# Kernel optimization log

Hardware: AMD Instinct MI355X
Metric: run time of the kernel (lower is better)

Reference implementation:

```python
import jax, jax.numpy as jnp
import numpy as np

N = 50000   # num_nodes
E = 800000  # num_edges (avg degree 16)
IN, H, OUT = 256, 128, 64
L = 4       # num_layers


def setup_inputs() -> dict:
    key = jax.random.key(0)
    ks = jax.random.split(key, 6)
    x = jax.random.normal(ks[0], (N, IN), jnp.float32)
    edge_index = jax.random.randint(ks[1], (2, E), 0, N, dtype=jnp.int64)
    W1 = jax.random.normal(ks[2], (IN, H), jnp.float32) / np.float32(np.sqrt(IN))
    b1 = jnp.zeros((H,), jnp.float32)
    Wr = jax.random.normal(ks[3], (L, H, H), jnp.float32) / np.float32(np.sqrt(H))
    eps = jnp.zeros((L,), jnp.float32)  # epsilons init to 0 as in the module
    W2 = jax.random.normal(ks[4], (H, OUT), jnp.float32) / np.float32(np.sqrt(H))
    b2 = jnp.zeros((OUT,), jnp.float32)
    return {"x": x, "W1": W1, "b1": b1, "Wr": Wr, "eps": eps,
            "W2": W2, "b2": b2, "edge_index": edge_index}


def reference(x, W1, b1, Wr, eps, W2, b2, edge_index):
    n = x.shape[0]
    # add self loops (done once in __init__ of the torch module)
    sl = jnp.arange(n, dtype=edge_index.dtype)
    row = jnp.concatenate([edge_index[0], sl])
    col = jnp.concatenate([edge_index[1], sl])
    # sym-normalized adjacency A_hat = D^-1/2 (A + I) D^-1/2; L_sym = I - A_hat
    deg = jax.ops.segment_sum(jnp.ones(row.shape, x.dtype), row, num_segments=n)
    dinv = jnp.where(deg > 0, jax.lax.rsqrt(deg), jnp.zeros_like(deg))
    w = dinv[row] * dinv[col]  # [E+N]

    def ahat(h):  # A_hat @ h via gather + segment scatter-add
        return jax.ops.segment_sum(w[:, None] * h[col], row, num_segments=n)

    h = jax.nn.relu(x @ W1 + b1)  # lin1 + ReLU (dropout = identity at eval)
    h0 = h
    for layer in range(Wr.shape[0]):
        h = h @ Wr[layer].T                 # lin_right (bias-free)
        h = 6.0 * h - 3.0 * ahat(h)         # 3 * (I + L_sym) @ h
        h0 = (1.0 + jnp.tanh(eps[layer])) * h0 + h  # epsilon-gated residual
        h = jax.nn.relu(h0)
    return h @ W2 + b2  # lin2 logits
```

## Files before the change

kernel.cpp:

```cpp
#include <hip/hip_runtime.h>
#include <math.h>


#define GBLK 256

typedef __bf16 bf16x8 __attribute__((ext_vector_type(8)));
typedef float f32x4 __attribute__((ext_vector_type(4)));
typedef unsigned int uint32x4 __attribute__((ext_vector_type(4)));

__device__ __forceinline__ ushort f2bf(float f) {
  unsigned u = __float_as_uint(f);
  return (ushort)((u + 0x7fffu + ((u >> 16) & 1u)) >> 16);
}

__global__ void k_count(const int* __restrict__ eidx, int* __restrict__ degi, int E, int n) {
  int e = blockIdx.x * blockDim.x + threadIdx.x;
  if (e < E) {
    int r = eidx[e];
    if ((unsigned)r < (unsigned)n) atomicAdd(&degi[r], 1);
  }
}

__global__ __launch_bounds__(1024) void k_scan1(const int* __restrict__ degi,
                                                int* __restrict__ rowstart,
                                                int* __restrict__ bsum, int n) {
  __shared__ int sm[1024];
  int tid = threadIdx.x;
  int i = blockIdx.x * 1024 + tid;
  int v = (i < n) ? degi[i] : 0;
  sm[tid] = v;
  __syncthreads();
  #pragma unroll
  for (int off = 1; off < 1024; off <<= 1) {
    int t = (tid >= off) ? sm[tid - off] : 0;
    __syncthreads();
    sm[tid] += t;
    __syncthreads();
  }
  if (i < n) rowstart[i] = sm[tid] - v;
  if (tid == 1023) bsum[blockIdx.x] = sm[1023];
}

__global__ void k_scan2(const int* __restrict__ bsum, int* __restrict__ boff, int nb) {
  if (threadIdx.x == 0 && blockIdx.x == 0) {
    int s = 0;
    for (int b = 0; b < nb; ++b) { boff[b] = s; s += bsum[b]; }
  }
}

__global__ __launch_bounds__(1024) void k_scan3(int* __restrict__ rowstart,
                                                const int* __restrict__ boff,
                                                int* __restrict__ cursor, int n, int E) {
  int i = blockIdx.x * 1024 + threadIdx.x;
  if (i < n) {
    int v = rowstart[i] + boff[blockIdx.x];
    rowstart[i] = v;
    cursor[i] = v;
  }
  if (i == 0) rowstart[n] = E;
}

__global__ void k_dinv(const int* __restrict__ degi, float* __restrict__ dinv, int n) {
  int i = blockIdx.x * blockDim.x + threadIdx.x;
  if (i < n) dinv[i] = rsqrtf((float)degi[i] + 1.0f);
}

__global__ void k_fill(const int* __restrict__ eidx, int* __restrict__ cursor,
                       int* __restrict__ colidx, int E, int n) {
  int e = blockIdx.x * blockDim.x + threadIdx.x;
  if (e < E) {
    int r = eidx[e];
    int c = eidx[E + e];
    if ((unsigned)r < (unsigned)n && (unsigned)c < (unsigned)n) {
      int pos = atomicAdd(&cursor[r], 1);
      colidx[pos] = c;
    }
  }
}

__global__ void k_cvt(const float* __restrict__ Wr, const float* __restrict__ W1,
                      const float* __restrict__ W2, ushort* __restrict__ wr_bf,
                      ushort* __restrict__ w1t, ushort* __restrict__ w2t,
                      int nwr, int nw1, int nw2) {
  int i = blockIdx.x * blockDim.x + threadIdx.x;
  if (i < nwr) {
    wr_bf[i] = f2bf(Wr[i]);
  } else if (i < nwr + nw1) {
    int m = i - nwr;
    int k = m >> 7, j = m & 127;
    w1t[j * 256 + k] = f2bf(W1[m]);
  } else if (i < nwr + nw1 + nw2) {
    int m = i - nwr - nw1;
    int k = m >> 6, j = m & 63;
    w2t[j * 128 + k] = f2bf(W2[m]);
  }
}

template <int K, int NOUT, bool AF32, int EPI>
__global__ __launch_bounds__(256) void mfma_gemm(const void* __restrict__ Ap,
                                                 const ushort* __restrict__ Bt,
                                                 const float* __restrict__ bias,
                                                 const float* __restrict__ dinv,
                                                 ushort* __restrict__ out_bf,
                                                 float* __restrict__ out_f32,
                                                 int n) {
  constexpr int KS = K / 32;
  constexpr int NT = NOUT / 16;
  const int lane = threadIdx.x & 63;
  const int wave = threadIdx.x >> 6;
  const int l15 = lane & 15;
  const int kq = lane >> 4;
  const int rowA = blockIdx.x * 64 + wave * 16 + l15;
  const bool arow_ok = rowA < n;

  f32x4 acc[NT];
  #pragma unroll
  for (int t = 0; t < NT; ++t) acc[t] = (f32x4){0.f, 0.f, 0.f, 0.f};

  #pragma unroll
  for (int kk = 0; kk < KS; ++kk) {
    bf16x8 a;
    if constexpr (AF32) {
      const float* A = (const float*)Ap;
      float4 f0 = make_float4(0.f, 0.f, 0.f, 0.f);
      float4 f1 = make_float4(0.f, 0.f, 0.f, 0.f);
      if (arow_ok) {
        f0 = *(const float4*)&A[(size_t)rowA * K + kk * 32 + kq * 8];
        f1 = *(const float4*)&A[(size_t)rowA * K + kk * 32 + kq * 8 + 4];
      }
      uint32x4 u;
      u[0] = (unsigned)f2bf(f0.x) | ((unsigned)f2bf(f0.y) << 16);
      u[1] = (unsigned)f2bf(f0.z) | ((unsigned)f2bf(f0.w) << 16);
      u[2] = (unsigned)f2bf(f1.x) | ((unsigned)f2bf(f1.y) << 16);
      u[3] = (unsigned)f2bf(f1.z) | ((unsigned)f2bf(f1.w) << 16);
      a = __builtin_bit_cast(bf16x8, u);
    } else {
      const ushort* A = (const ushort*)Ap;
      uint32x4 u = (uint32x4){0u, 0u, 0u, 0u};
      if (arow_ok) u = *(const uint32x4*)&A[(size_t)rowA * K + kk * 32 + kq * 8];
      a = __builtin_bit_cast(bf16x8, u);
    }
    #pragma unroll
    for (int t = 0; t < NT; ++t) {
      uint32x4 ub = *(const uint32x4*)&Bt[(size_t)(t * 16 + l15) * K + kk * 32 + kq * 8];
      bf16x8 b = __builtin_bit_cast(bf16x8, ub);
      acc[t] = __builtin_amdgcn_mfma_f32_16x16x32_bf16(a, b, acc[t], 0, 0, 0);
    }
  }

  const int rbase = blockIdx.x * 64 + wave * 16 + kq * 4;

  float bcol[NT];
  #pragma unroll
  for (int t = 0; t < NT; ++t) {
    if constexpr (EPI != 1) bcol[t] = bias[t * 16 + l15];
    else bcol[t] = 0.f;
  }
  float sc[4];
  #pragma unroll
  for (int r = 0; r < 4; ++r) {
    if constexpr (EPI == 1) sc[r] = (rbase + r < n) ? dinv[rbase + r] : 0.f;
    else sc[r] = 0.f;
  }

  #pragma unroll
  for (int r = 0; r < 4; ++r) {
    int row = rbase + r;
    if (row < n) {
      #pragma unroll
      for (int t = 0; t < NT; ++t) {
        int col = t * 16 + l15;
        float v = acc[t][r];
        if constexpr (EPI == 0) {
          v += bcol[t];
          v = fmaxf(v, 0.f);
          out_bf[(size_t)row * NOUT + col] = f2bf(v);
          out_f32[(size_t)row * NOUT + col] = v;
        } else if constexpr (EPI == 1) {
          out_bf[(size_t)row * NOUT + col] = f2bf(v * sc[r]);
        } else {
          out_f32[(size_t)row * NOUT + col] = v + bcol[t];
        }
      }
    }
  }
}

__global__ __launch_bounds__(256) void k_spmm2(const ushort* __restrict__ pre,
                                               const float* __restrict__ dinv,
                                               const int* __restrict__ rowstart,
                                               const int* __restrict__ colidx,
                                               const float* __restrict__ eps, int layer,
                                               float* __restrict__ h0,
                                               ushort* __restrict__ hbf, int n) {
  const int lane = threadIdx.x & 63;
  const int r = blockIdx.x * 4 + (threadIdx.x >> 6);
  if (r >= n) return;

  const int s0 = rowstart[r], s1 = rowstart[r + 1];
  const float dr = dinv[r];

  const size_t rowoff = (size_t)r * 128 + lane * 2;
  const unsigned ur = *(const unsigned*)&pre[rowoff];
  const float2 h0v = *(const float2*)&h0[rowoff];

  float accx = 0.f, accy = 0.f;
  for (int base = s0; base < s1; base += 64) {
    int m = s1 - base; if (m > 64) m = 64;
    int ci = 0;
    if (base + lane < s1) ci = colidx[base + lane];
    int e = 0;
    for (; e + 3 < m; e += 4) {
      int c0 = __shfl(ci, e);
      int c1 = __shfl(ci, e + 1);
      int c2 = __shfl(ci, e + 2);
      int c3 = __shfl(ci, e + 3);
      unsigned u0 = *(const unsigned*)&pre[(size_t)c0 * 128 + lane * 2];
      unsigned u1 = *(const unsigned*)&pre[(size_t)c1 * 128 + lane * 2];
      unsigned u2 = *(const unsigned*)&pre[(size_t)c2 * 128 + lane * 2];
      unsigned u3 = *(const unsigned*)&pre[(size_t)c3 * 128 + lane * 2];
      accx += __uint_as_float(u0 << 16);
      accy += __uint_as_float(u0 & 0xffff0000u);
      accx += __uint_as_float(u1 << 16);
      accy += __uint_as_float(u1 & 0xffff0000u);
      accx += __uint_as_float(u2 << 16);
      accy += __uint_as_float(u2 & 0xffff0000u);
      accx += __uint_as_float(u3 << 16);
      accy += __uint_as_float(u3 & 0xffff0000u);
    }
    for (; e < m; ++e) {
      int c = __shfl(ci, e);
      unsigned u = *(const unsigned*)&pre[(size_t)c * 128 + lane * 2];
      accx += __uint_as_float(u << 16);
      accy += __uint_as_float(u & 0xffff0000u);
    }
  }

  const float p0 = __uint_as_float(ur << 16);
  const float p1 = __uint_as_float(ur & 0xffff0000u);
  const float a = (6.0f - 3.0f * dr * dr) / dr;
  const float m3dr = -3.0f * dr;
  const float g = 1.0f + tanhf(eps[layer]);

  float v0 = g * h0v.x + a * p0 + m3dr * accx;
  float v1 = g * h0v.y + a * p1 + m3dr * accy;
  *(float2*)&h0[rowoff] = make_float2(v0, v1);
  unsigned hb = (unsigned)f2bf(fmaxf(v0, 0.f)) | ((unsigned)f2bf(fmaxf(v1, 0.f)) << 16);
  *(unsigned*)&hbf[rowoff] = hb;
}

extern "C" void kernel_launch(void* const* d_in, const int* in_sizes, int n_in,
                              void* d_out, int out_size, void* d_ws, size_t ws_size,
                              hipStream_t stream) {
  const float* x   = (const float*)d_in[0];
  const float* W1  = (const float*)d_in[1];
  const float* b1  = (const float*)d_in[2];
  const float* Wr  = (const float*)d_in[3];
  const float* eps = (const float*)d_in[4];
  const float* W2  = (const float*)d_in[5];
  const float* b2  = (const float*)d_in[6];
  const int*   eidx= (const int*)d_in[7];

  const int IN = 256, H = 128, OUT = 64;
  const int n = in_sizes[0] / IN;
  const int E = in_sizes[7] / 2;
  const int L = in_sizes[4];

  size_t off = 0;
  auto carve = [&](size_t bytes) -> void* {
    void* p = (char*)d_ws + off;
    off += (bytes + 255) & ~(size_t)255;
    return p;
  };
  int*    degi     = (int*)carve((size_t)n * 4);
  int*    rowstart = (int*)carve((size_t)(n + 1) * 4);
  int*    cursor   = (int*)carve((size_t)n * 4);
  int*    bsum     = (int*)carve(64 * 4);
  int*    boff     = (int*)carve(64 * 4);
  int*    colidx   = (int*)carve((size_t)E * 4);
  float*  dinv     = (float*)carve((size_t)n * 4);
  float*  h0       = (float*)carve((size_t)n * H * 4);
  ushort* hbf      = (ushort*)carve((size_t)n * H * 2);
  ushort* pre      = (ushort*)carve((size_t)n * H * 2);
  ushort* wr_bf    = (ushort*)carve((size_t)L * H * H * 2);
  ushort* w1t      = (ushort*)carve((size_t)IN * H * 2);
  ushort* w2t      = (ushort*)carve((size_t)H * OUT * 2);
  if (off > ws_size) return;

  hipMemsetAsync(degi, 0, (size_t)n * 4, stream);
  k_count<<<(E + 255) / 256, 256, 0, stream>>>(eidx, degi, E, n);
  int nwr = L * H * H, nw1 = IN * H, nw2 = H * OUT;
  k_cvt<<<(nwr + nw1 + nw2 + 255) / 256, 256, 0, stream>>>(Wr, W1, W2, wr_bf, w1t, w2t,
                                                           nwr, nw1, nw2);
  int nb = (n + 1023) / 1024;
  k_scan1<<<nb, 1024, 0, stream>>>(degi, rowstart, bsum, n);
  k_scan2<<<1, 64, 0, stream>>>(bsum, boff, nb);
  k_scan3<<<nb, 1024, 0, stream>>>(rowstart, boff, cursor, n, E);
  k_dinv<<<(n + 255) / 256, 256, 0, stream>>>(degi, dinv, n);
  k_fill<<<(E + 255) / 256, 256, 0, stream>>>(eidx, cursor, colidx, E, n);

  int gx = (n + 63) / 64;
  mfma_gemm<256, 128, true, 0><<<gx, 256, 0, stream>>>(x, w1t, b1, nullptr, hbf, h0, n);
  for (int l = 0; l < L; ++l) {
    mfma_gemm<128, 128, false, 1><<<gx, 256, 0, stream>>>(
        hbf, wr_bf + (size_t)l * H * H, nullptr, dinv, pre, nullptr, n);
    k_spmm2<<<(n + 3) / 4, 256, 0, stream>>>(pre, dinv, rowstart, colidx, eps, l, h0, hbf, n);
  }
  mfma_gemm<128, 64, false, 2><<<gx, 256, 0, stream>>>(hbf, w2t, b2, nullptr, nullptr,
                                                       (float*)d_out, n);
}
```

Measured before the change: 494.5 us.

## Store residual in bf16, use 16-bit column indices, widen SpMM gathers

Keeps the epsilon-gated residual h0 in bf16 rather than fp32, with layer 0 reading it from the ReLU'd bf16 hidden buffer. This halves residual read/write traffic in every layer. Column indices are stored as 16-bit when the node count fits, and the SpMM splits each wavefront into two halves that gather 8-byte vectors from alternate neighbours, then combine with a shuffle. The dinv computation is fused into the scan kernel. The trade-off is reduced precision in the residual accumulation across layers, plus a code path that depends on node count.

```diff
diff --git a/kernel.cpp b/kernel.cpp
--- a/kernel.cpp
+++ b/kernel.cpp
@@ -1,8 +1,6 @@
 #include <hip/hip_runtime.h>
 #include <math.h>
 
-
-#define GBLK 256
 
 typedef __bf16 bf16x8 __attribute__((ext_vector_type(8)));
 typedef float f32x4 __attribute__((ext_vector_type(4)));
@@ -12,6 +10,8 @@
   unsigned u = __float_as_uint(f);
   return (ushort)((u + 0x7fffu + ((u >> 16) & 1u)) >> 16);
 }
+__device__ __forceinline__ float bflo(unsigned u) { return __uint_as_float(u << 16); }
+__device__ __forceinline__ float bfhi(unsigned u) { return __uint_as_float(u & 0xffff0000u); }
 
 __global__ void k_count(const int* __restrict__ eidx, int* __restrict__ degi, int E, int n) {
   int e = blockIdx.x * blockDim.x + threadIdx.x;
@@ -50,30 +50,29 @@
 
 __global__ __launch_bounds__(1024) void k_scan3(int* __restrict__ rowstart,
                                                 const int* __restrict__ boff,
-                                                int* __restrict__ cursor, int n, int E) {
+                                                int* __restrict__ cursor,
+                                                const int* __restrict__ degi,
+                                                float* __restrict__ dinv, int n, int E) {
   int i = blockIdx.x * 1024 + threadIdx.x;
   if (i < n) {
     int v = rowstart[i] + boff[blockIdx.x];
     rowstart[i] = v;
     cursor[i] = v;
+    dinv[i] = rsqrtf((float)degi[i] + 1.0f);
   }
   if (i == 0) rowstart[n] = E;
 }
 
-__global__ void k_dinv(const int* __restrict__ degi, float* __restrict__ dinv, int n) {
-  int i = blockIdx.x * blockDim.x + threadIdx.x;
-  if (i < n) dinv[i] = rsqrtf((float)degi[i] + 1.0f);
-}
-
+template <typename IDX>
 __global__ void k_fill(const int* __restrict__ eidx, int* __restrict__ cursor,
-                       int* __restrict__ colidx, int E, int n) {
+                       IDX* __restrict__ colidx, int E, int n) {
   int e = blockIdx.x * blockDim.x + threadIdx.x;
   if (e < E) {
     int r = eidx[e];
     int c = eidx[E + e];
     if ((unsigned)r < (unsigned)n && (unsigned)c < (unsigned)n) {
       int pos = atomicAdd(&cursor[r], 1);
-      colidx[pos] = c;
+      colidx[pos] = (IDX)c;
     }
   }
 }
@@ -175,7 +174,6 @@
           v += bcol[t];
           v = fmaxf(v, 0.f);
           out_bf[(size_t)row * NOUT + col] = f2bf(v);
-          out_f32[(size_t)row * NOUT + col] = v;
         } else if constexpr (EPI == 1) {
           out_bf[(size_t)row * NOUT + col] = f2bf(v * sc[r]);
         } else {
@@ -186,12 +184,14 @@
   }
 }
 
-__global__ __launch_bounds__(256) void k_spmm2(const ushort* __restrict__ pre,
+template <typename IDX>
+__global__ __launch_bounds__(256) void k_spmm3(const ushort* __restrict__ pre,
                                                const float* __restrict__ dinv,
                                                const int* __restrict__ rowstart,
-                                               const int* __restrict__ colidx,
+                                               const IDX* __restrict__ colidx,
                                                const float* __restrict__ eps, int layer,
-                                               float* __restrict__ h0,
+                                               const ushort* __restrict__ h0in,
+                                               ushort* __restrict__ h0out,
                                                ushort* __restrict__ hbf, int n) {
   const int lane = threadIdx.x & 63;
   const int r = blockIdx.x * 4 + (threadIdx.x >> 6);
@@ -199,54 +199,68 @@
 
   const int s0 = rowstart[r], s1 = rowstart[r + 1];
   const float dr = dinv[r];
-
-  const size_t rowoff = (size_t)r * 128 + lane * 2;
-  const unsigned ur = *(const unsigned*)&pre[rowoff];
-  const float2 h0v = *(const float2*)&h0[rowoff];
-
-  float accx = 0.f, accy = 0.f;
+  const int half = lane >> 5;
+  const int c4 = lane & 31;
+  const size_t rowb = (size_t)r * 128 + c4 * 4;
+
+  const uint2 pr = *(const uint2*)&pre[rowb];
+  const uint2 h0u = *(const uint2*)&h0in[rowb];
+
+  float a0 = 0.f, a1 = 0.f, a2 = 0.f, a3 = 0.f;
   for (int base = s0; base < s1; base += 64) {
     int m = s1 - base; if (m > 64) m = 64;
     int ci = 0;
-    if (base + lane < s1) ci = colidx[base + lane];
-    int e = 0;
-    for (; e + 3 < m; e += 4) {
-      int c0 = __shfl(ci, e);
-      int c1 = __shfl(ci, e + 1);
-      int c2 = __shfl(ci, e + 2);
-      int c3 = __shfl(ci, e + 3);
-      unsigned u0 = *(const unsigned*)&pre[(size_t)c0 * 128 + lane * 2];
-      unsigned u1 = *(const unsigned*)&pre[(size_t)c1 * 128 + lane * 2];
-      unsigned u2 = *(const unsigned*)&pre[(size_t)c2 * 128 + lane * 2];
-      unsigned u3 = *(const unsigned*)&pre[(size_t)c3 * 128 + lane * 2];
-      accx += __uint_as_float(u0 << 16);
-      accy += __uint_as_float(u0 & 0xffff0000u);
-      accx += __uint_as_float(u1 << 16);
-      accy += __uint_as_float(u1 & 0xffff0000u);
-      accx += __uint_as_float(u2 << 16);
-      accy += __uint_as_float(u2 & 0xffff0000u);
-      accx += __uint_as_float(u3 << 16);
-      accy += __uint_as_float(u3 & 0xffff0000u);
-    }
-    for (; e < m; ++e) {
-      int c = __shfl(ci, e);
-      unsigned u = *(const unsigned*)&pre[(size_t)c * 128 + lane * 2];
-      accx += __uint_as_float(u << 16);
-      accy += __uint_as_float(u & 0xffff0000u);
-    }
-  }
-
-  const float p0 = __uint_as_float(ur << 16);
-  const float p1 = __uint_as_float(ur & 0xffff0000u);
-  const float a = (6.0f - 3.0f * dr * dr) / dr;
-  const float m3dr = -3.0f * dr;
-  const float g = 1.0f + tanhf(eps[layer]);
-
-  float v0 = g * h0v.x + a * p0 + m3dr * accx;
-  float v1 = g * h0v.y + a * p1 + m3dr * accy;
-  *(float2*)&h0[rowoff] = make_float2(v0, v1);
-  unsigned hb = (unsigned)f2bf(fmaxf(v0, 0.f)) | ((unsigned)f2bf(fmaxf(v1, 0.f)) << 16);
-  *(unsigned*)&hbf[rowoff] = hb;
+    if (base + lane < s1) ci = (int)colidx[base + lane];
+    int full = m >> 1;
+    int i = 0;
+    for (; i + 3 < full; i += 4) {
+      int cA = __shfl(ci, 2 * i + half);
+      int cB = __shfl(ci, 2 * i + 2 + half);
+      int cC = __shfl(ci, 2 * i + 4 + half);
+      int cD = __shfl(ci, 2 * i + 6 + half);
+      uint2 uA = *(const uint2*)&pre[(size_t)cA * 128 + c4 * 4];
+      uint2 uB = *(const uint2*)&pre[(size_t)cB * 128 + c4 * 4];
+      uint2 uC = *(const uint2*)&pre[(size_t)cC * 128 + c4 * 4];
+      uint2 uD = *(const uint2*)&pre[(size_t)cD * 128 + c4 * 4];
+      a0 += bflo(uA.x); a1 += bfhi(uA.x); a2 += bflo(uA.y); a3 += bfhi(uA.y);
+      a0 += bflo(uB.x); a1 += bfhi(uB.x); a2 += bflo(uB.y); a3 += bfhi(uB.y);
+      a0 += bflo(uC.x); a1 += bfhi(uC.x); a2 += bflo(uC.y); a3 += bfhi(uC.y);
+      a0 += bflo(uD.x); a1 += bfhi(uD.x); a2 += bflo(uD.y); a3 += bfhi(uD.y);
+    }
+    for (; i < full; ++i) {
+      int cA = __shfl(ci, 2 * i + half);
+      uint2 uA = *(const uint2*)&pre[(size_t)cA * 128 + c4 * 4];
+      a0 += bflo(uA.x); a1 += bfhi(uA.x); a2 += bflo(uA.y); a3 += bfhi(uA.y);
+    }
+    if (m & 1) {
+      int cZ = __shfl(ci, m - 1);
+      if (half == 0) {
+        uint2 uZ = *(const uint2*)&pre[(size_t)cZ * 128 + c4 * 4];
+        a0 += bflo(uZ.x); a1 += bfhi(uZ.x); a2 += bflo(uZ.y); a3 += bfhi(uZ.y);
+      }
+    }
+  }
+  a0 += __shfl_xor(a0, 32);
+  a1 += __shfl_xor(a1, 32);
+  a2 += __shfl_xor(a2, 32);
+  a3 += __shfl_xor(a3, 32);
+
+  if (half == 0) {
+    const float aa = (6.0f - 3.0f * dr * dr) / dr;
+    const float m3 = -3.0f * dr;
+    const float g = 1.0f + tanhf(eps[layer]);
+    float v0 = g * bflo(h0u.x) + aa * bflo(pr.x) + m3 * a0;
+    float v1 = g * bfhi(h0u.x) + aa * bfhi(pr.x) + m3 * a1;
+    float v2 = g * bflo(h0u.y) + aa * bflo(pr.y) + m3 * a2;
+    float v3 = g * bfhi(h0u.y) + aa * bfhi(pr.y) + m3 * a3;
+    uint2 ho, hr;
+    ho.x = (unsigned)f2bf(v0) | ((unsigned)f2bf(v1) << 16);
+    ho.y = (unsigned)f2bf(v2) | ((unsigned)f2bf(v3) << 16);
+    hr.x = (unsigned)f2bf(fmaxf(v0, 0.f)) | ((unsigned)f2bf(fmaxf(v1, 0.f)) << 16);
+    hr.y = (unsigned)f2bf(fmaxf(v2, 0.f)) | ((unsigned)f2bf(fmaxf(v3, 0.f)) << 16);
+    *(uint2*)&h0out[rowb] = ho;
+    *(uint2*)&hbf[rowb] = hr;
+  }
 }
 
 extern "C" void kernel_launch(void* const* d_in, const int* in_sizes, int n_in,
@@ -277,15 +291,17 @@
   int*    cursor   = (int*)carve((size_t)n * 4);
   int*    bsum     = (int*)carve(64 * 4);
   int*    boff     = (int*)carve(64 * 4);
-  int*    colidx   = (int*)carve((size_t)E * 4);
+  void*   colidx   = carve((size_t)E * 4);
   float*  dinv     = (float*)carve((size_t)n * 4);
-  float*  h0       = (float*)carve((size_t)n * H * 4);
+  ushort* h0bf     = (ushort*)carve((size_t)n * H * 2);
   ushort* hbf      = (ushort*)carve((size_t)n * H * 2);
   ushort* pre      = (ushort*)carve((size_t)n * H * 2);
   ushort* wr_bf    = (ushort*)carve((size_t)L * H * H * 2);
   ushort* w1t      = (ushort*)carve((size_t)IN * H * 2);
   ushort* w2t      = (ushort*)carve((size_t)H * OUT * 2);
   if (off > ws_size) return;
+
+  const bool small = (n < 65536);
 
   hipMemsetAsync(degi, 0, (size_t)n * 4, stream);
   k_count<<<(E + 255) / 256, 256, 0, stream>>>(eidx, degi, E, n);
@@ -295,16 +311,24 @@
   int nb = (n + 1023) / 1024;
   k_scan1<<<nb, 1024, 0, stream>>>(degi, rowstart, bsum, n);
   k_scan2<<<1, 64, 0, stream>>>(bsum, boff, nb);
-  k_scan3<<<nb, 1024, 0, stream>>>(rowstart, boff, cursor, n, E);
-  k_dinv<<<(n + 255) / 256, 256, 0, stream>>>(degi, dinv, n);
-  k_fill<<<(E + 255) / 256, 256, 0, stream>>>(eidx, cursor, colidx, E, n);
+  k_scan3<<<nb, 1024, 0, stream>>>(rowstart, boff, cursor, degi, dinv, n, E);
+  if (small)
+    k_fill<ushort><<<(E + 255) / 256, 256, 0, stream>>>(eidx, cursor, (ushort*)colidx, E, n);
+  else
+    k_fill<int><<<(E + 255) / 256, 256, 0, stream>>>(eidx, cursor, (int*)colidx, E, n);
 
   int gx = (n + 63) / 64;
-  mfma_gemm<256, 128, true, 0><<<gx, 256, 0, stream>>>(x, w1t, b1, nullptr, hbf, h0, n);
+  mfma_gemm<256, 128, true, 0><<<gx, 256, 0, stream>>>(x, w1t, b1, nullptr, hbf, nullptr, n);
   for (int l = 0; l < L; ++l) {
     mfma_gemm<128, 128, false, 1><<<gx, 256, 0, stream>>>(
         hbf, wr_bf + (size_t)l * H * H, nullptr, dinv, pre, nullptr, n);
-    k_spmm2<<<(n + 3) / 4, 256, 0, stream>>>(pre, dinv, rowstart, colidx, eps, l, h0, hbf, n);
+    const ushort* h0in = (l == 0) ? hbf : h0bf;
+    if (small)
+      k_spmm3<ushort><<<(n + 3) / 4, 256, 0, stream>>>(pre, dinv, rowstart,
+          (const ushort*)colidx, eps, l, h0in, h0bf, hbf, n);
+    else
+      k_spmm3<int><<<(n + 3) / 4, 256, 0, stream>>>(pre, dinv, rowstart,
+          (const int*)colidx, eps, l, h0in, h0bf, hbf, n);
   }
   mfma_gemm<128, 64, false, 2><<<gx, 256, 0, stream>>>(hbf, w2t, b2, nullptr, nullptr,
                                                        (float*)d_out, n);
```

Result: faster. 465.0 us (-6.0%).
